# Kernel tuning notes

Hardware: AMD Instinct MI355X
Metric: run time of the kernel (lower is better)

Reference implementation:

```python
import jax, jax.numpy as jnp
import numpy as np
import math

MODEL_DIM = 1024
HEAD_DIM = 64
NUM_HEADS = 16
FF_MULT = 4
FF_DIM = FF_MULT * MODEL_DIM
ATTN_DIM = NUM_HEADS * HEAD_DIM
FUSED_DIMS = (ATTN_DIM, ATTN_DIM, ATTN_DIM, FF_DIM, FF_DIM)


def setup_inputs() -> dict:
    key = jax.random.key(0)
    k_x, k_in, k_attn, k_ff = jax.random.split(key, 4)
    B, S = 2, 2048
    inputs = jax.random.normal(k_x, (B, S, MODEL_DIM), dtype=jnp.float32)
    # LayerNorm affine params (torch defaults: weight=1, bias=0)
    ln_w = jnp.ones((MODEL_DIM,), dtype=jnp.float32)
    ln_b = jnp.zeros((MODEL_DIM,), dtype=jnp.float32)
    # Linear weights stored as [in, out] (equivalent to torch W.T)
    s_in = 1.0 / math.sqrt(MODEL_DIM)
    w_in = jax.random.uniform(k_in, (MODEL_DIM, sum(FUSED_DIMS)), jnp.float32, -s_in, s_in)
    s_a = 1.0 / math.sqrt(ATTN_DIM)
    w_attn = jax.random.uniform(k_attn, (ATTN_DIM, MODEL_DIM), jnp.float32, -s_a, s_a)
    s_f = 1.0 / math.sqrt(FF_DIM)
    w_ff = jax.random.uniform(k_ff, (FF_DIM, MODEL_DIM), jnp.float32, -s_f, s_f)
    return {"inputs": inputs, "ln_w": ln_w, "ln_b": ln_b,
            "w_in": w_in, "w_attn": w_attn, "w_ff": w_ff}


def _layer_norm(x, w, b, eps=1e-5):
    mu = jnp.mean(x, axis=-1, keepdims=True)
    var = jnp.var(x, axis=-1, keepdims=True)
    return (x - mu) * jax.lax.rsqrt(var + eps) * w + b


def reference(inputs, ln_w, ln_b, w_in, w_attn, w_ff):
    B, S, D = inputs.shape
    units = _layer_norm(inputs, ln_w, ln_b)
    proj = units @ w_in                                   # [B,S,3*A+2*F]
    splits = np.cumsum(FUSED_DIMS)[:-1]
    q, k, v, ff, ff_gate = jnp.split(proj, splits, axis=-1)
    # split heads: [B,S,H*d] -> [B,H,S,d]
    def heads(t):
        return t.reshape(B, S, NUM_HEADS, HEAD_DIM).transpose(0, 2, 1, 3)
    q, k, v = heads(q), heads(k), heads(v)
    scale = 1.0 / math.sqrt(HEAD_DIM)
    score = jnp.einsum('bhsd,bhTd->bhsT', q, k) * scale   # [B,H,S,S]
    weight = jax.nn.softmax(score, axis=-1)
    attn = jnp.einsum('bhsT,bhTd->bhsd', weight, v)       # [B,H,S,d]
    concat = attn.transpose(0, 2, 1, 3).reshape(B, S, ATTN_DIM)
    attn_out = concat @ w_attn                            # [B,S,D]
    ff_out = (ff * jax.nn.gelu(ff_gate, approximate=True)) @ w_ff
    return inputs + attn_out + ff_out
```

## Files before the change

### kernel.cpp

```cpp
#include <hip/hip_runtime.h>
#include <hip/hip_bf16.h>
#include <cstdint>
#include <cstddef>

typedef __bf16 bf16;
typedef __bf16 bf16x8 __attribute__((ext_vector_type(8)));
typedef float f32x4 __attribute__((ext_vector_type(4)));

#define MFMA16(a, b, c) __builtin_amdgcn_mfma_f32_16x16x32_bf16(a, b, c, 0, 0, 0)

#define GLOBAL_LOAD_LDS16(gptr, lptr)                                          \
  __builtin_amdgcn_global_load_lds(                                            \
      (const __attribute__((address_space(1))) void*)(gptr),                   \
      (__attribute__((address_space(3))) void*)(lptr), 16, 0, 0)

__global__ void transpose_all(const float* __restrict__ w_in,
                              const float* __restrict__ w_attn,
                              const float* __restrict__ w_ff,
                              bf16* __restrict__ wt_in,
                              bf16* __restrict__ wtcat) {
  __shared__ float t[32][33];
  int id = blockIdx.x;
  const float* src; bf16* dst;
  int srcN, srccol0, LDO, mode, obase, goff, kcol0, ntn;
  if (id < 3072) {
    src = w_in; dst = wt_in; srcN = 11264; srccol0 = 0; LDO = 1024;
    mode = 0; obase = 0; goff = 0; kcol0 = 0; ntn = 96;
  } else if (id < 7168) {
    id -= 3072; src = w_in; dst = wt_in; srcN = 11264; srccol0 = 3072;
    LDO = 1024; mode = 1; obase = 3072; goff = 0; kcol0 = 0; ntn = 128;
  } else if (id < 11264) {
    id -= 7168; src = w_in; dst = wt_in; srcN = 11264; srccol0 = 7168;
    LDO = 1024; mode = 1; obase = 3072; goff = 64; kcol0 = 0; ntn = 128;
  } else if (id < 12288) {
    id -= 11264; src = w_attn; dst = wtcat; srcN = 1024; srccol0 = 0;
    LDO = 5120; mode = 0; obase = 0; goff = 0; kcol0 = 0; ntn = 32;
  } else {
    id -= 12288; src = w_ff; dst = wtcat; srcN = 1024; srccol0 = 0;
    LDO = 5120; mode = 0; obase = 0; goff = 0; kcol0 = 1024; ntn = 32;
  }
  const int n0 = (id % ntn) * 32, k0 = (id / ntn) * 32;
  const int tx = threadIdx.x, ty = threadIdx.y;
  for (int i = ty; i < 32; i += 8)
    t[i][tx] = src[(size_t)(k0 + i) * srcN + srccol0 + n0 + tx];
  __syncthreads();
  for (int i = ty; i < 32; i += 8) {
    int n = n0 + i;
    int orow = mode ? (obase + ((n >> 6) << 7) + goff + (n & 63)) : (obase + n);
    dst[(size_t)orow * LDO + kcol0 + k0 + tx] = (bf16)t[tx][i];
  }
}

__global__ __launch_bounds__(256) void lnorm(const float* __restrict__ x,
                                             const float* __restrict__ w,
                                             const float* __restrict__ b,
                                             bf16* __restrict__ y) {
  const int row = blockIdx.x;
  const int tid = threadIdx.x;
  const float* xr = x + (size_t)row * 1024;
  float4 v = *(const float4*)&xr[tid * 4];
  float s = v.x + v.y + v.z + v.w;
  float ss = v.x * v.x + v.y * v.y + v.z * v.z + v.w * v.w;
  __shared__ float rs[256], rss[256];
  rs[tid] = s; rss[tid] = ss;
  __syncthreads();
  for (int off = 128; off > 0; off >>= 1) {
    if (tid < off) { rs[tid] += rs[tid + off]; rss[tid] += rss[tid + off]; }
    __syncthreads();
  }
  const float mean = rs[0] * (1.f / 1024.f);
  const float var = rss[0] * (1.f / 1024.f) - mean * mean;
  const float rstd = rsqrtf(var + 1e-5f);
  const float* vp = (const float*)&v;
  for (int i = 0; i < 4; i++) {
    int c = tid * 4 + i;
    y[(size_t)row * 1024 + c] = (bf16)((vp[i] - mean) * rstd * w[c] + b[c]);
  }
}

__global__ __launch_bounds__(256) void vtrans(const bf16* __restrict__ proj,
                                              bf16* __restrict__ vt) {
  __shared__ bf16 t[64][80];
  const int tid = threadIdx.x;
  const int s0 = blockIdx.x * 64;
  const int h = blockIdx.y, b = blockIdx.z;
  constexpr size_t LDP = 3072;
  const bf16* src = proj + (size_t)b * 2048 * LDP + 2048 + h * 64;
  {
    int s = tid >> 2, d0 = (tid & 3) * 16;
    *(bf16x8*)&t[s][d0]     = *(const bf16x8*)&src[(size_t)(s0 + s) * LDP + d0];
    *(bf16x8*)&t[s][d0 + 8] = *(const bf16x8*)&src[(size_t)(s0 + s) * LDP + d0 + 8];
  }
  __syncthreads();
  {
    int d = tid >> 2, sb = (tid & 3) * 16;
    bf16* dst = vt + ((size_t)(b * 16 + h) * 64 + d) * 2048 + s0 + sb;
    bf16x8 o0, o1;
    for (int i = 0; i < 8; i++) { o0[i] = t[sb + i][d]; o1[i] = t[sb + 8 + i][d]; }
    *(bf16x8*)&dst[0] = o0;
    *(bf16x8*)&dst[8] = o1;
  }
}

__global__ __launch_bounds__(256) void flash_attn(const bf16* __restrict__ proj,
                                                  const bf16* __restrict__ vt,
                                                  bf16* __restrict__ hcat) {
  __shared__ __align__(16) char smem[50176];
  bf16* Ks = (bf16*)smem;
  bf16* Vs = (bf16*)(smem + 16384);
  bf16* Ps = (bf16*)(smem + 32768);
  const int tid = threadIdx.x;
  const int wave = tid >> 6, lane = tid & 63;
  const int quad = lane >> 4, l16 = lane & 15;
  const int q0 = blockIdx.x * 64;
  const int h = blockIdx.y, b = blockIdx.z;
  constexpr size_t LDP = 3072;
  const bf16* Qb = proj + (size_t)b * 2048 * LDP + h * 64;
  const bf16* Kb = proj + (size_t)b * 2048 * LDP + 1024 + h * 64;
  const bf16* Vt = vt + (size_t)(b * 16 + h) * 64 * 2048;

  const int qrow = q0 + wave * 16 + l16;
  bf16x8 aq0r = *(const bf16x8*)&Qb[(size_t)qrow * LDP + quad * 8];
  bf16x8 aq1r = *(const bf16x8*)&Qb[(size_t)qrow * LDP + 32 + quad * 8];
  bf16x8 aq0, aq1;
#pragma unroll
  for (int i = 0; i < 8; i++) {
    aq0[i] = (bf16)((float)aq0r[i] * 0.125f);
    aq1[i] = (bf16)((float)aq1r[i] * 0.125f);
  }

  f32x4 O[4] = {};
  float lrow[4] = {0.f, 0.f, 0.f, 0.f};

  const int krow_ = wave * 8 + (lane >> 3);
  const int kq_ = ((lane & 7) ^ (krow_ & 7)) * 8;
  const int vrow_ = wave * 4 + (lane >> 4);
  const int vq_ = ((lane & 15) ^ (vrow_ & 15)) * 8;
  const int ks0 = (quad ^ (l16 & 7)) * 8;
  const int ks1 = ((quad + 4) ^ (l16 & 7)) * 8;

  for (int j0 = 0; j0 < 2048; j0 += 128) {
#pragma unroll
    for (int p = 0; p < 4; p++) {
      int kr = p * 32 + krow_;
      GLOBAL_LOAD_LDS16(&Kb[(size_t)(j0 + kr) * LDP + kq_],
                        &Ks[kr * 64 + (lane & 7) * 8]);
      int vr = p * 16 + vrow_;
      GLOBAL_LOAD_LDS16(&Vt[(size_t)vr * 2048 + j0 + vq_],
                        &Vs[vr * 128 + (lane & 15) * 8]);
    }
    __syncthreads();

    f32x4 sa[8];
#pragma unroll
    for (int nt = 0; nt < 8; nt++) {
      int r = nt * 16 + l16;
      bf16x8 bk0 = *(const bf16x8*)&Ks[r * 64 + (quad ^ (r & 7)) * 8];
      bf16x8 bk1 = *(const bf16x8*)&Ks[r * 64 + ((quad + 4) ^ (r & 7)) * 8];
      f32x4 t = {};
      t = MFMA16(aq0, bk0, t);
      sa[nt] = MFMA16(aq1, bk1, t);
    }

    bf16* Pw = Ps + wave * (16 * 136);
#pragma unroll
    for (int r = 0; r < 4; r++) {
      bf16* pr = &Pw[(quad * 4 + r) * 136];
      float ts = 0.f;
#pragma unroll
      for (int nt = 0; nt < 8; nt++) {
        float p = __expf(sa[nt][r]);
        pr[nt * 16 + l16] = (bf16)p;
        ts += p;
      }
#pragma unroll
      for (int d = 1; d < 16; d <<= 1) ts += __shfl_xor(ts, d, 64);
      lrow[r] += ts;
    }

#pragma unroll
    for (int kg = 0; kg < 4; kg++) {
      bf16x8 aP = *(const bf16x8*)&Pw[l16 * 136 + kg * 32 + quad * 8];
#pragma unroll
      for (int nb = 0; nb < 4; nb++) {
        int vrr = nb * 16 + l16;
        int vsl = ((kg * 4 + quad) ^ (vrr & 15)) * 8;
        bf16x8 bv = *(const bf16x8*)&Vs[vrr * 128 + vsl];
        O[nb] = MFMA16(aP, bv, O[nb]);
      }
    }
    __syncthreads();
  }

#pragma unroll
  for (int r = 0; r < 4; r++) {
    float inv = 1.f / lrow[r];
    size_t row = (size_t)b * 2048 + q0 + wave * 16 + quad * 4 + r;
#pragma unroll
    for (int nb = 0; nb < 4; nb++)
      hcat[row * 5120 + h * 64 + nb * 16 + l16] = (bf16)(O[nb][r] * inv);
  }
}

__global__ __launch_bounds__(256) void gemm_proj(const bf16* __restrict__ A,
                                                 const bf16* __restrict__ Bt,
                                                 bf16* __restrict__ proj,
                                                 bf16* __restrict__ hcat) {
  constexpr int K = 1024, LDC = 136;
  __shared__ __align__(16) char smem[32768];
  bf16* As = (bf16*)smem;
  bf16* Bs = As + 128 * 64;
  bf16* Cs = (bf16*)smem;
  const int tid = threadIdx.x;
  const int wave = tid >> 6, lane = tid & 63;
  const int quad = lane >> 4, l16 = lane & 15;
  constexpr int NM = 4, NN = 4;
  const int wm0 = (wave >> 1) * 64, wn0 = (wave & 1) * 64;
  const size_t rowA0 = (size_t)blockIdx.y * 128;
  const size_t rowB0 = (size_t)blockIdx.x * 128;

  const int srow = tid >> 3;
  const int sq = ((tid & 7) ^ (srow & 7)) * 8;
  const int sslot = (tid & 7) * 8;

  f32x4 acc[NM][NN] = {};

  for (int k0 = 0; k0 < K; k0 += 64) {
#pragma unroll
    for (int p = 0; p < 4; p++) {
      int r = p * 32 + srow;
      GLOBAL_LOAD_LDS16(&A[(rowA0 + r) * K + k0 + sq], &As[r * 64 + sslot]);
      GLOBAL_LOAD_LDS16(&Bt[(rowB0 + r) * K + k0 + sq], &Bs[r * 64 + sslot]);
    }
    __syncthreads();
#pragma unroll
    for (int c = 0; c < 2; c++) {
      bf16x8 af[NM], bfr[NN];
#pragma unroll
      for (int i = 0; i < NM; i++) {
        int r = wm0 + i * 16 + l16;
        af[i] = *(const bf16x8*)&As[r * 64 + ((c * 4 + quad) ^ (r & 7)) * 8];
      }
#pragma unroll
      for (int j = 0; j < NN; j++) {
        int r = wn0 + j * 16 + l16;
        bfr[j] = *(const bf16x8*)&Bs[r * 64 + ((c * 4 + quad) ^ (r & 7)) * 8];
      }
#pragma unroll
      for (int i = 0; i < NM; i++)
#pragma unroll
        for (int j = 0; j < NN; j++)
          acc[i][j] = MFMA16(af[i], bfr[j], acc[i][j]);
    }
    __syncthreads();
  }

#pragma unroll
  for (int half = 0; half < 2; half++) {
    if ((wave >> 1) == half) {
#pragma unroll
      for (int i = 0; i < NM; i++)
#pragma unroll
        for (int j = 0; j < NN; j++)
#pragma unroll
          for (int r = 0; r < 4; r++)
            Cs[(i * 16 + quad * 4 + r) * LDC + wn0 + j * 16 + l16] =
                (bf16)acc[i][j][r];
    }
    __syncthreads();
    if (blockIdx.x < 24) {
      const int c0 = (tid & 15) * 8;
#pragma unroll
      for (int it = 0; it < 4; it++) {
        int row = (tid >> 4) + it * 16;
        *(bf16x8*)&proj[(rowA0 + half * 64 + row) * 3072 + rowB0 + c0] =
            *(const bf16x8*)&Cs[row * LDC + c0];
      }
    } else {
      const int T = blockIdx.x - 24;
      const int c0 = (tid & 7) * 8;
#pragma unroll
      for (int p = 0; p < 2; p++) {
        int row = (tid >> 3) + p * 32;
        bf16x8 f = *(const bf16x8*)&Cs[row * LDC + c0];
        bf16x8 g = *(const bf16x8*)&Cs[row * LDC + 64 + c0];
        bf16x8 o;
#pragma unroll
        for (int i = 0; i < 8; i++) {
          float xg = (float)g[i];
          float u = 0.7978845608f * (xg + 0.044715f * xg * xg * xg);
          float gl = xg / (1.f + __expf(-2.f * u));
          o[i] = (bf16)((float)f[i] * gl);
        }
        *(bf16x8*)&hcat[(rowA0 + half * 64 + row) * 5120 + 1024 + T * 64 + c0] = o;
      }
    }
    __syncthreads();
  }
}

__global__ __launch_bounds__(256) void gemm_out(const bf16* __restrict__ A,
                                                const bf16* __restrict__ Bt,
                                                bf16* __restrict__ part) {
  constexpr int LDAB = 5120, LDC = 136;
  __shared__ __align__(16) char smem[32768];
  bf16* As = (bf16*)smem;
  bf16* Bs = As + 128 * 64;
  bf16* Cs = (bf16*)smem;
  const int tid = threadIdx.x;
  const int wave = tid >> 6, lane = tid & 63;
  const int quad = lane >> 4, l16 = lane & 15;
  constexpr int NM = 4, NN = 4;
  const int wm0 = (wave >> 1) * 64, wn0 = (wave & 1) * 64;
  const size_t rowA0 = (size_t)blockIdx.y * 128;
  const size_t rowB0 = (size_t)blockIdx.x * 128;
  const int kbeg = blockIdx.z * 1280, kend = kbeg + 1280;

  const int srow = tid >> 3;
  const int sq = ((tid & 7) ^ (srow & 7)) * 8;
  const int sslot = (tid & 7) * 8;

  f32x4 acc[NM][NN] = {};

  for (int k0 = kbeg; k0 < kend; k0 += 64) {
#pragma unroll
    for (int p = 0; p < 4; p++) {
      int r = p * 32 + srow;
      GLOBAL_LOAD_LDS16(&A[(rowA0 + r) * LDAB + k0 + sq], &As[r * 64 + sslot]);
      GLOBAL_LOAD_LDS16(&Bt[(rowB0 + r) * LDAB + k0 + sq], &Bs[r * 64 + sslot]);
    }
    __syncthreads();
#pragma unroll
    for (int c = 0; c < 2; c++) {
      bf16x8 af[NM], bfr[NN];
#pragma unroll
      for (int i = 0; i < NM; i++) {
        int r = wm0 + i * 16 + l16;
        af[i] = *(const bf16x8*)&As[r * 64 + ((c * 4 + quad) ^ (r & 7)) * 8];
      }
#pragma unroll
      for (int j = 0; j < NN; j++) {
        int r = wn0 + j * 16 + l16;
        bfr[j] = *(const bf16x8*)&Bs[r * 64 + ((c * 4 + quad) ^ (r & 7)) * 8];
      }
#pragma unroll
      for (int i = 0; i < NM; i++)
#pragma unroll
        for (int j = 0; j < NN; j++)
          acc[i][j] = MFMA16(af[i], bfr[j], acc[i][j]);
    }
    __syncthreads();
  }

  bf16* dst = part + (size_t)blockIdx.z * (4096 * 1024);
#pragma unroll
  for (int half = 0; half < 2; half++) {
    if ((wave >> 1) == half) {
#pragma unroll
      for (int i = 0; i < NM; i++)
#pragma unroll
        for (int j = 0; j < NN; j++)
#pragma unroll
          for (int r = 0; r < 4; r++)
            Cs[(i * 16 + quad * 4 + r) * LDC + wn0 + j * 16 + l16] =
                (bf16)acc[i][j][r];
    }
    __syncthreads();
    const int c0 = (tid & 15) * 8;
#pragma unroll
    for (int it = 0; it < 4; it++) {
      int row = (tid >> 4) + it * 16;
      *(bf16x8*)&dst[(rowA0 + half * 64 + row) * 1024 + rowB0 + c0] =
          *(const bf16x8*)&Cs[row * LDC + c0];
    }
    __syncthreads();
  }
}

__global__ __launch_bounds__(256) void reduce_out(const float* __restrict__ x,
                                                  const bf16* __restrict__ part,
                                                  float* __restrict__ out) {
  const size_t i = ((size_t)blockIdx.x * 256 + threadIdx.x) * 8;
  constexpr size_t SL = 4096 * 1024;
  float r[8];
  float4 x0 = *(const float4*)&x[i];
  float4 x1 = *(const float4*)&x[i + 4];
  r[0] = x0.x; r[1] = x0.y; r[2] = x0.z; r[3] = x0.w;
  r[4] = x1.x; r[5] = x1.y; r[6] = x1.z; r[7] = x1.w;
#pragma unroll
  for (int z = 0; z < 4; z++) {
    bf16x8 p = *(const bf16x8*)&part[z * SL + i];
#pragma unroll
    for (int k = 0; k < 8; k++) r[k] += (float)p[k];
  }
  float4 o0 = {r[0], r[1], r[2], r[3]};
  float4 o1 = {r[4], r[5], r[6], r[7]};
  *(float4*)&out[i] = o0;
  *(float4*)&out[i + 4] = o1;
}

extern "C" void kernel_launch(void* const* d_in, const int* in_sizes, int n_in,
                              void* d_out, int out_size, void* d_ws, size_t ws_size,
                              hipStream_t stream) {
  const float* x      = (const float*)d_in[0];
  const float* ln_w   = (const float*)d_in[1];
  const float* ln_b   = (const float*)d_in[2];
  const float* w_in   = (const float*)d_in[3];
  const float* w_attn = (const float*)d_in[4];
  const float* w_ff   = (const float*)d_in[5];
  float* out = (float*)d_out;
  char* ws = (char*)d_ws;

  bf16* wt_in = (bf16*)(ws);
  bf16* wtcat = (bf16*)(ws + 23068672);
  bf16* xn    = (bf16*)(ws + 33554432);
  bf16* proj  = (bf16*)(ws + 41943040);
  bf16* part  = (bf16*)(ws + 67108864);
  bf16* vt    = (bf16*)(ws + 100663296);
  bf16* hcat  = (bf16*)(ws + 134217728);

  transpose_all<<<16384, dim3(32, 8), 0, stream>>>(w_in, w_attn, w_ff, wt_in, wtcat);
  lnorm<<<4096, 256, 0, stream>>>(x, ln_w, ln_b, xn);
  gemm_proj<<<dim3(88, 32), 256, 0, stream>>>(xn, wt_in, proj, hcat);
  vtrans<<<dim3(32, 16, 2), 256, 0, stream>>>(proj, vt);
  flash_attn<<<dim3(32, 16, 2), 256, 0, stream>>>(proj, vt, hcat);
  gemm_out<<<dim3(8, 32, 4), 256, 0, stream>>>(hcat, wtcat, part);
  reduce_out<<<2048, 256, 0, stream>>>(x, part, out);
}
```

Before: 426.6 us.

## Merge weight transpose and layernorm launches, shrink projection K-tile, defer row-sum shuffles

Merges the weight-transpose and layernorm kernels into one launch that picks its role by block index, removing one kernel launch and its gap. Halves the projection GEMM K-tile from 64 to 32 with a matching XOR swizzle, cutting its LDS use from 32KB to 17KB. The smaller footprint allows more resident blocks, at the cost of twice as many barriers per K loop. In flash attention, the cross-lane row-sum shuffle reduction moves out of the inner loop and runs once at the end.

After: 399.4 us. -6.4%, faster.

```diff
diff --git a/kernel.cpp b/kernel.cpp
--- a/kernel.cpp
+++ b/kernel.cpp
@@ -14,67 +14,70 @@
       (const __attribute__((address_space(1))) void*)(gptr),                   \
       (__attribute__((address_space(3))) void*)(lptr), 16, 0, 0)
 
-__global__ void transpose_all(const float* __restrict__ w_in,
-                              const float* __restrict__ w_attn,
-                              const float* __restrict__ w_ff,
-                              bf16* __restrict__ wt_in,
-                              bf16* __restrict__ wtcat) {
-  __shared__ float t[32][33];
-  int id = blockIdx.x;
-  const float* src; bf16* dst;
-  int srcN, srccol0, LDO, mode, obase, goff, kcol0, ntn;
-  if (id < 3072) {
-    src = w_in; dst = wt_in; srcN = 11264; srccol0 = 0; LDO = 1024;
-    mode = 0; obase = 0; goff = 0; kcol0 = 0; ntn = 96;
-  } else if (id < 7168) {
-    id -= 3072; src = w_in; dst = wt_in; srcN = 11264; srccol0 = 3072;
-    LDO = 1024; mode = 1; obase = 3072; goff = 0; kcol0 = 0; ntn = 128;
-  } else if (id < 11264) {
-    id -= 7168; src = w_in; dst = wt_in; srcN = 11264; srccol0 = 7168;
-    LDO = 1024; mode = 1; obase = 3072; goff = 64; kcol0 = 0; ntn = 128;
-  } else if (id < 12288) {
-    id -= 11264; src = w_attn; dst = wtcat; srcN = 1024; srccol0 = 0;
-    LDO = 5120; mode = 0; obase = 0; goff = 0; kcol0 = 0; ntn = 32;
+__global__ __launch_bounds__(256) void prep(const float* __restrict__ w_in,
+                                            const float* __restrict__ w_attn,
+                                            const float* __restrict__ w_ff,
+                                            bf16* __restrict__ wt_in,
+                                            bf16* __restrict__ wtcat,
+                                            const float* __restrict__ x,
+                                            const float* __restrict__ ln_w,
+                                            const float* __restrict__ ln_b,
+                                            bf16* __restrict__ xn) {
+  __shared__ __align__(16) char sm[4352];
+  if (blockIdx.x < 16384) {
+    float(*t)[33] = (float(*)[33])sm;
+    int id = blockIdx.x;
+    const float* src; bf16* dst;
+    int srcN, srccol0, LDO, mode, obase, goff, kcol0, ntn;
+    if (id < 3072) {
+      src = w_in; dst = wt_in; srcN = 11264; srccol0 = 0; LDO = 1024;
+      mode = 0; obase = 0; goff = 0; kcol0 = 0; ntn = 96;
+    } else if (id < 7168) {
+      id -= 3072; src = w_in; dst = wt_in; srcN = 11264; srccol0 = 3072;
+      LDO = 1024; mode = 1; obase = 3072; goff = 0; kcol0 = 0; ntn = 128;
+    } else if (id < 11264) {
+      id -= 7168; src = w_in; dst = wt_in; srcN = 11264; srccol0 = 7168;
+      LDO = 1024; mode = 1; obase = 3072; goff = 64; kcol0 = 0; ntn = 128;
+    } else if (id < 12288) {
+      id -= 11264; src = w_attn; dst = wtcat; srcN = 1024; srccol0 = 0;
+      LDO = 5120; mode = 0; obase = 0; goff = 0; kcol0 = 0; ntn = 32;
+    } else {
+      id -= 12288; src = w_ff; dst = wtcat; srcN = 1024; srccol0 = 0;
+      LDO = 5120; mode = 0; obase = 0; goff = 0; kcol0 = 1024; ntn = 32;
+    }
+    const int n0 = (id % ntn) * 32, k0 = (id / ntn) * 32;
+    const int tx = threadIdx.x & 31, ty = threadIdx.x >> 5;
+    for (int i = ty; i < 32; i += 8)
+      t[i][tx] = src[(size_t)(k0 + i) * srcN + srccol0 + n0 + tx];
+    __syncthreads();
+    for (int i = ty; i < 32; i += 8) {
+      int n = n0 + i;
+      int orow = mode ? (obase + ((n >> 6) << 7) + goff + (n & 63)) : (obase + n);
+      dst[(size_t)orow * LDO + kcol0 + k0 + tx] = (bf16)t[tx][i];
+    }
   } else {
-    id -= 12288; src = w_ff; dst = wtcat; srcN = 1024; srccol0 = 0;
-    LDO = 5120; mode = 0; obase = 0; goff = 0; kcol0 = 1024; ntn = 32;
-  }
-  const int n0 = (id % ntn) * 32, k0 = (id / ntn) * 32;
-  const int tx = threadIdx.x, ty = threadIdx.y;
-  for (int i = ty; i < 32; i += 8)
-    t[i][tx] = src[(size_t)(k0 + i) * srcN + srccol0 + n0 + tx];
-  __syncthreads();
-  for (int i = ty; i < 32; i += 8) {
-    int n = n0 + i;
-    int orow = mode ? (obase + ((n >> 6) << 7) + goff + (n & 63)) : (obase + n);
-    dst[(size_t)orow * LDO + kcol0 + k0 + tx] = (bf16)t[tx][i];
-  }
-}
-
-__global__ __launch_bounds__(256) void lnorm(const float* __restrict__ x,
-                                             const float* __restrict__ w,
-                                             const float* __restrict__ b,
-                                             bf16* __restrict__ y) {
-  const int row = blockIdx.x;
-  const int tid = threadIdx.x;
-  const float* xr = x + (size_t)row * 1024;
-  float4 v = *(const float4*)&xr[tid * 4];
-  float s = v.x + v.y + v.z + v.w;
-  float ss = v.x * v.x + v.y * v.y + v.z * v.z + v.w * v.w;
-  __shared__ float rs[256], rss[256];
-  rs[tid] = s; rss[tid] = ss;
-  __syncthreads();
-  for (int off = 128; off > 0; off >>= 1) {
-    if (tid < off) { rs[tid] += rs[tid + off]; rss[tid] += rss[tid + off]; }
-    __syncthreads();
-  }
-  const float mean = rs[0] * (1.f / 1024.f);
-  const float var = rss[0] * (1.f / 1024.f) - mean * mean;
-  const float rstd = rsqrtf(var + 1e-5f);
-  const float* vp = (const float*)&v;
-  for (int i = 0; i < 4; i++) {
-    int c = tid * 4 + i;
-    y[(size_t)row * 1024 + c] = (bf16)((vp[i] - mean) * rstd * w[c] + b[c]);
+    float* rs = (float*)sm;
+    float* rss = rs + 256;
+    const int row = blockIdx.x - 16384;
+    const int tid = threadIdx.x;
+    const float* xr = x + (size_t)row * 1024;
+    float4 v = *(const float4*)&xr[tid * 4];
+    float s = v.x + v.y + v.z + v.w;
+    float ss = v.x * v.x + v.y * v.y + v.z * v.z + v.w * v.w;
+    rs[tid] = s; rss[tid] = ss;
+    __syncthreads();
+    for (int off = 128; off > 0; off >>= 1) {
+      if (tid < off) { rs[tid] += rs[tid + off]; rss[tid] += rss[tid + off]; }
+      __syncthreads();
+    }
+    const float mean = rs[0] * (1.f / 1024.f);
+    const float var = rss[0] * (1.f / 1024.f) - mean * mean;
+    const float rstd = rsqrtf(var + 1e-5f);
+    const float* vp = (const float*)&v;
+    for (int i = 0; i < 4; i++) {
+      int c = tid * 4 + i;
+      xn[(size_t)row * 1024 + c] = (bf16)((vp[i] - mean) * rstd * ln_w[c] + ln_b[c]);
+    }
   }
 }
 
@@ -130,14 +133,12 @@
   }
 
   f32x4 O[4] = {};
-  float lrow[4] = {0.f, 0.f, 0.f, 0.f};
+  float plrow[4] = {0.f, 0.f, 0.f, 0.f};
 
   const int krow_ = wave * 8 + (lane >> 3);
   const int kq_ = ((lane & 7) ^ (krow_ & 7)) * 8;
   const int vrow_ = wave * 4 + (lane >> 4);
   const int vq_ = ((lane & 15) ^ (vrow_ & 15)) * 8;
-  const int ks0 = (quad ^ (l16 & 7)) * 8;
-  const int ks1 = ((quad + 4) ^ (l16 & 7)) * 8;
 
   for (int j0 = 0; j0 < 2048; j0 += 128) {
 #pragma unroll
@@ -173,9 +174,7 @@
         pr[nt * 16 + l16] = (bf16)p;
         ts += p;
       }
-#pragma unroll
-      for (int d = 1; d < 16; d <<= 1) ts += __shfl_xor(ts, d, 64);
-      lrow[r] += ts;
+      plrow[r] += ts;
     }
 
 #pragma unroll
@@ -194,7 +193,10 @@
 
 #pragma unroll
   for (int r = 0; r < 4; r++) {
-    float inv = 1.f / lrow[r];
+    float ts = plrow[r];
+#pragma unroll
+    for (int d = 1; d < 16; d <<= 1) ts += __shfl_xor(ts, d, 64);
+    float inv = 1.f / ts;
     size_t row = (size_t)b * 2048 + q0 + wave * 16 + quad * 4 + r;
 #pragma unroll
     for (int nb = 0; nb < 4; nb++)
@@ -207,9 +209,9 @@
                                                  bf16* __restrict__ proj,
                                                  bf16* __restrict__ hcat) {
   constexpr int K = 1024, LDC = 136;
-  __shared__ __align__(16) char smem[32768];
+  __shared__ __align__(16) char smem[17408];
   bf16* As = (bf16*)smem;
-  bf16* Bs = As + 128 * 64;
+  bf16* Bs = As + 128 * 32;
   bf16* Cs = (bf16*)smem;
   const int tid = threadIdx.x;
   const int wave = tid >> 6, lane = tid & 63;
@@ -219,39 +221,33 @@
   const size_t rowA0 = (size_t)blockIdx.y * 128;
   const size_t rowB0 = (size_t)blockIdx.x * 128;
 
-  const int srow = tid >> 3;
-  const int sq = ((tid & 7) ^ (srow & 7)) * 8;
-  const int sslot = (tid & 7) * 8;
+  const int srow = wave * 16 + (lane >> 2);
+  const int sq = ((lane & 3) ^ ((lane >> 3) & 3)) * 8;
+  const int sslot = (lane & 3) * 8;
+  const int rslot = (quad ^ ((l16 >> 1) & 3)) * 8;
 
   f32x4 acc[NM][NN] = {};
 
-  for (int k0 = 0; k0 < K; k0 += 64) {
-#pragma unroll
-    for (int p = 0; p < 4; p++) {
-      int r = p * 32 + srow;
-      GLOBAL_LOAD_LDS16(&A[(rowA0 + r) * K + k0 + sq], &As[r * 64 + sslot]);
-      GLOBAL_LOAD_LDS16(&Bt[(rowB0 + r) * K + k0 + sq], &Bs[r * 64 + sslot]);
-    }
-    __syncthreads();
-#pragma unroll
-    for (int c = 0; c < 2; c++) {
-      bf16x8 af[NM], bfr[NN];
-#pragma unroll
-      for (int i = 0; i < NM; i++) {
-        int r = wm0 + i * 16 + l16;
-        af[i] = *(const bf16x8*)&As[r * 64 + ((c * 4 + quad) ^ (r & 7)) * 8];
-      }
-#pragma unroll
-      for (int j = 0; j < NN; j++) {
-        int r = wn0 + j * 16 + l16;
-        bfr[j] = *(const bf16x8*)&Bs[r * 64 + ((c * 4 + quad) ^ (r & 7)) * 8];
-      }
-#pragma unroll
-      for (int i = 0; i < NM; i++)
-#pragma unroll
-        for (int j = 0; j < NN; j++)
-          acc[i][j] = MFMA16(af[i], bfr[j], acc[i][j]);
-    }
+  for (int k0 = 0; k0 < K; k0 += 32) {
+#pragma unroll
+    for (int p = 0; p < 2; p++) {
+      int r = p * 64 + srow;
+      GLOBAL_LOAD_LDS16(&A[(rowA0 + r) * K + k0 + sq], &As[r * 32 + sslot]);
+      GLOBAL_LOAD_LDS16(&Bt[(rowB0 + r) * K + k0 + sq], &Bs[r * 32 + sslot]);
+    }
+    __syncthreads();
+    bf16x8 af[NM], bfr[NN];
+#pragma unroll
+    for (int i = 0; i < NM; i++)
+      af[i] = *(const bf16x8*)&As[(wm0 + i * 16 + l16) * 32 + rslot];
+#pragma unroll
+    for (int j = 0; j < NN; j++)
+      bfr[j] = *(const bf16x8*)&Bs[(wn0 + j * 16 + l16) * 32 + rslot];
+#pragma unroll
+    for (int i = 0; i < NM; i++)
+#pragma unroll
+      for (int j = 0; j < NN; j++)
+        acc[i][j] = MFMA16(af[i], bfr[j], acc[i][j]);
     __syncthreads();
   }
 
@@ -419,8 +415,8 @@
   bf16* vt    = (bf16*)(ws + 100663296);
   bf16* hcat  = (bf16*)(ws + 134217728);
 
-  transpose_all<<<16384, dim3(32, 8), 0, stream>>>(w_in, w_attn, w_ff, wt_in, wtcat);
-  lnorm<<<4096, 256, 0, stream>>>(x, ln_w, ln_b, xn);
+  prep<<<20480, 256, 0, stream>>>(w_in, w_attn, w_ff, wt_in, wtcat,
+                                  x, ln_w, ln_b, xn);
   gemm_proj<<<dim3(88, 32), 256, 0, stream>>>(xn, wt_in, proj, hcat);
   vtrans<<<dim3(32, 16, 2), 256, 0, stream>>>(proj, vt);
   flash_attn<<<dim3(32, 16, 2), 256, 0, stream>>>(proj, vt, hcat);
```
